# Performance work log

Measured on AMD Instinct MI355X. Metric: run time of the kernel, lower is better.

Reference implementation:

```python
import jax, jax.numpy as jnp
import numpy as np

N, F_IN, F_HID, N_HEADS, F_OUT, ALPHA = 4096, 128, 64, 4, 64, 0.2
AVG_DEG = 32.0


def setup_inputs() -> dict:
    key = jax.random.key(0)
    ks = jax.random.split(key, 8)
    x = jax.random.normal(ks[0], (N, F_IN), dtype=jnp.float32)
    # sparse-ish adjacency (avg degree ~32) + self loops so every row has a neighbor
    adj = (jax.random.uniform(ks[1], (N, N)) < (AVG_DEG / N)).astype(jnp.float32)
    adj = jnp.maximum(adj, jnp.eye(N, dtype=jnp.float32))
    s = 1.0 / np.sqrt(F_IN)
    lin_W = jax.random.uniform(ks[2], (F_IN, F_IN), jnp.float32, -s, s)
    lin_b = jax.random.uniform(ks[3], (F_IN,), jnp.float32, -s, s)
    W_heads = jax.random.normal(ks[4], (N_HEADS, F_IN, F_HID), jnp.float32) * 0.1
    a_heads = jax.random.normal(ks[5], (N_HEADS, 2 * F_HID), jnp.float32) * 0.1
    W_end = jax.random.normal(ks[6], (N_HEADS * F_HID, F_OUT), jnp.float32) * 0.1
    a_end = jax.random.normal(ks[7], (2 * F_OUT,), jnp.float32) * 0.1
    return dict(x=x, adj=adj, lin_W=lin_W, lin_b=lin_b,
                W_heads=W_heads, a_heads=a_heads, W_end=W_end, a_end=a_end)


def _gat_layer(h, adj, W, a):
    # standard dense-masked GAT layer (pyGAT style)
    Wh = h @ W                      # [N, F']
    f = W.shape[1]
    src = Wh @ a[:f]                # [N]  a^T contribution of source node
    dst = Wh @ a[f:]                # [N]  contribution of destination node
    e = jax.nn.leaky_relu(src[:, None] + dst[None, :], ALPHA)  # [N, N]
    e = jnp.where(adj > 0, e, -9e15)
    att = jax.nn.softmax(e, axis=1)  # neighbor softmax per row
    return jax.nn.elu(att @ Wh)      # [N, F']


def reference(x, adj, lin_W, lin_b, W_heads, a_heads, W_end, a_end):
    h = x @ lin_W + lin_b            # nn.Linear(input_features, input_features)
    # parallel multi-head attention, then concat along feature dim
    heads = jax.vmap(lambda W, a: _gat_layer(h, adj, W, a))(W_heads, a_heads)  # [H, N, F_HID]
    hcat = jnp.transpose(heads, (1, 0, 2)).reshape(N, N_HEADS * F_HID)         # [N, H*F_HID]
    out = _gat_layer(hcat, adj, W_end, a_end)                                  # [N, F_OUT]
    return jax.nn.softmax(out, axis=1)
```

## Files before the change

kernel.cpp:

```cpp
#include <hip/hip_runtime.h>

#define GN 4096
#define F_IN 128
#define F_HID 64
#define NHEADS 4
#define F_OUT 64
#define ALPHA 0.2f
#define NGEMM 512

#define OFF_WH     0
#define OFF_SRC1   4194304
#define OFF_DST1   4259840
#define OFF_WH2    4325376
#define OFF_SRC2   5373952
#define OFF_DST2   5390336
#define OFF_BM     5406720

__global__ __launch_bounds__(256) void prep_kernel(
        const float* __restrict__ adj, const float* __restrict__ x,
        const float* __restrict__ linW, const float* __restrict__ linb,
        const float* __restrict__ Wheads, const float* __restrict__ aheads,
        float* __restrict__ Wh, float* __restrict__ src1, float* __restrict__ dst1,
        unsigned short* __restrict__ bm) {
    __shared__ struct { float xs[8][128]; float hs[8][128]; } sm;
    const int tid = threadIdx.x;

    if (blockIdx.x >= NGEMM) {
        const int row = blockIdx.x - NGEMM;
        const float4* a4 = (const float4*)(adj + (size_t)row * GN) + tid * 4;
        float4 v0 = a4[0], v1 = a4[1], v2 = a4[2], v3 = a4[3];
        unsigned msk = 0;
        msk |= (v0.x > 0.0f) ? 1u : 0u;         msk |= (v0.y > 0.0f) ? 2u : 0u;
        msk |= (v0.z > 0.0f) ? 4u : 0u;         msk |= (v0.w > 0.0f) ? 8u : 0u;
        msk |= (v1.x > 0.0f) ? 16u : 0u;        msk |= (v1.y > 0.0f) ? 32u : 0u;
        msk |= (v1.z > 0.0f) ? 64u : 0u;        msk |= (v1.w > 0.0f) ? 128u : 0u;
        msk |= (v2.x > 0.0f) ? 256u : 0u;       msk |= (v2.y > 0.0f) ? 512u : 0u;
        msk |= (v2.z > 0.0f) ? 1024u : 0u;      msk |= (v2.w > 0.0f) ? 2048u : 0u;
        msk |= (v3.x > 0.0f) ? 4096u : 0u;      msk |= (v3.y > 0.0f) ? 8192u : 0u;
        msk |= (v3.z > 0.0f) ? 16384u : 0u;     msk |= (v3.w > 0.0f) ? 32768u : 0u;
        bm[row * 256 + tid] = (unsigned short)msk;
        return;
    }

    const int i0 = blockIdx.x * 8;
    #pragma unroll
    for (int t = 0; t < 4; ++t) {
        int e = t * 256 + tid;
        sm.xs[e >> 7][e & 127] = x[(size_t)i0 * 128 + e];
    }
    __syncthreads();
    {
        const int k = tid & 127;
        const int n0 = tid >> 7;
        float bk = linb[k];
        float a0 = bk, a1 = bk, a2 = bk, a3 = bk;
        for (int j = 0; j < 128; ++j) {
            float w = linW[j * 128 + k];
            a0 += sm.xs[n0][j] * w;
            a1 += sm.xs[n0 + 2][j] * w;
            a2 += sm.xs[n0 + 4][j] * w;
            a3 += sm.xs[n0 + 6][j] * w;
        }
        sm.hs[n0][k] = a0; sm.hs[n0 + 2][k] = a1;
        sm.hs[n0 + 4][k] = a2; sm.hs[n0 + 6][k] = a3;
    }
    __syncthreads();
    {
        const int hd = tid >> 6, f = tid & 63;
        float acc[8] = {0, 0, 0, 0, 0, 0, 0, 0};
        const float* Wp = Wheads + (size_t)hd * F_IN * F_HID + f;
        for (int j = 0; j < 128; ++j) {
            float w = Wp[j * 64];
            #pragma unroll
            for (int n = 0; n < 8; ++n) acc[n] += sm.hs[n][j] * w;
        }
        const float as = aheads[hd * 128 + f];
        const float ad = aheads[hd * 128 + 64 + f];
        #pragma unroll
        for (int n = 0; n < 8; ++n) {
            Wh[(size_t)(i0 + n) * 256 + hd * 64 + f] = acc[n];
            float sv = acc[n] * as, dv = acc[n] * ad;
            #pragma unroll
            for (int o = 32; o > 0; o >>= 1) {
                sv += __shfl_xor(sv, o, 64);
                dv += __shfl_xor(dv, o, 64);
            }
            if (f == 0) { src1[(i0 + n) * 4 + hd] = sv; dst1[(i0 + n) * 4 + hd] = dv; }
        }
    }
}

__device__ __forceinline__ int build_row_nbrs(const unsigned short* __restrict__ bm,
                                              int row, int lane, int* sidx) {
    unsigned long long bits =
        ((const unsigned long long*)(bm + (size_t)row * 256))[lane];
    int c = __popcll(bits);
    int inc = c;
    #pragma unroll
    for (int o = 1; o < 64; o <<= 1) {
        int n = __shfl_up(inc, o, 64);
        if (lane >= o) inc += n;
    }
    int p = inc - c;
    const int deg = __shfl(inc, 63, 64);
    const int col0 = lane * 64;
    while (bits) {
        int k = __ffsll((long long)bits) - 1;
        if (p < 136) sidx[p] = col0 + k;
        ++p;
        bits &= bits - 1;
    }
    const int deg4 = (deg + 3) & ~3;
    if (lane < deg4 - deg) sidx[deg + lane] = 0;
    return deg;
}

__global__ __launch_bounds__(256) void attn_mid_kernel(
        const float* __restrict__ Wh, const float* __restrict__ src1,
        const float* __restrict__ dst1, const float* __restrict__ Wend,
        const float* __restrict__ aend, float* __restrict__ Wh2,
        float* __restrict__ src2, float* __restrict__ dst2,
        const unsigned short* __restrict__ bm) {
    __shared__ float ps[4][528];
    __shared__ float hcat[4][256];
    __shared__ int   sidx[4][136];
    const int wave = threadIdx.x >> 6;
    const int lane = threadIdx.x & 63;
    const int row  = blockIdx.x * 4 + wave;

    const int deg = build_row_nbrs(bm, row, lane, sidx[wave]);
    const int* nb = sidx[wave];
    const int nchunk = (deg + 63) >> 6;

    const float4 s4 = ((const float4*)src1)[row];
    float4 ev[2];
    float4 m4 = make_float4(-1e30f, -1e30f, -1e30f, -1e30f);
    for (int c = 0; c < nchunk; ++c) {
        int t = c * 64 + lane;
        float4 e = make_float4(-1e30f, -1e30f, -1e30f, -1e30f);
        if (t < deg) {
            int j = nb[t];
            float4 d = ((const float4*)dst1)[j];
            e.x = s4.x + d.x; e.x = (e.x > 0.0f) ? e.x : ALPHA * e.x;
            e.y = s4.y + d.y; e.y = (e.y > 0.0f) ? e.y : ALPHA * e.y;
            e.z = s4.z + d.z; e.z = (e.z > 0.0f) ? e.z : ALPHA * e.z;
            e.w = s4.w + d.w; e.w = (e.w > 0.0f) ? e.w : ALPHA * e.w;
        }
        ev[c] = e;
        m4.x = fmaxf(m4.x, e.x); m4.y = fmaxf(m4.y, e.y);
        m4.z = fmaxf(m4.z, e.z); m4.w = fmaxf(m4.w, e.w);
    }
    #pragma unroll
    for (int o = 32; o > 0; o >>= 1) {
        m4.x = fmaxf(m4.x, __shfl_xor(m4.x, o, 64));
        m4.y = fmaxf(m4.y, __shfl_xor(m4.y, o, 64));
        m4.z = fmaxf(m4.z, __shfl_xor(m4.z, o, 64));
        m4.w = fmaxf(m4.w, __shfl_xor(m4.w, o, 64));
    }
    float4 l4 = make_float4(0.f, 0.f, 0.f, 0.f);
    for (int c = 0; c < nchunk; ++c) {
        ev[c].x = expf(ev[c].x - m4.x); l4.x += ev[c].x;
        ev[c].y = expf(ev[c].y - m4.y); l4.y += ev[c].y;
        ev[c].z = expf(ev[c].z - m4.z); l4.z += ev[c].z;
        ev[c].w = expf(ev[c].w - m4.w); l4.w += ev[c].w;
    }
    #pragma unroll
    for (int o = 32; o > 0; o >>= 1) {
        l4.x += __shfl_xor(l4.x, o, 64);
        l4.y += __shfl_xor(l4.y, o, 64);
        l4.z += __shfl_xor(l4.z, o, 64);
        l4.w += __shfl_xor(l4.w, o, 64);
    }
    const float4 inv = make_float4(1.f / l4.x, 1.f / l4.y, 1.f / l4.z, 1.f / l4.w);
    for (int c = 0; c < nchunk; ++c) {
        int t = c * 64 + lane;
        float4 p = make_float4(ev[c].x * inv.x, ev[c].y * inv.y,
                               ev[c].z * inv.z, ev[c].w * inv.w);
        ((float4*)&ps[wave][0])[t] = p;
    }

    const int hl = lane >> 4;
    const float4* Wh4 = (const float4*)Wh;
    float4 acc = make_float4(0.f, 0.f, 0.f, 0.f);
    const int deg4 = (deg + 3) & ~3;
    for (int t = 0; t < deg4; t += 4) {
        int4 jj = *(const int4*)(nb + t);
        float4 w0 = Wh4[(size_t)jj.x * 64 + lane];
        float4 w1 = Wh4[(size_t)jj.y * 64 + lane];
        float4 w2 = Wh4[(size_t)jj.z * 64 + lane];
        float4 w3 = Wh4[(size_t)jj.w * 64 + lane];
        const float* pp = &ps[wave][t * 4 + hl];
        float p0 = pp[0], p1 = pp[4], p2 = pp[8], p3 = pp[12];
        acc.x += p0 * w0.x + p1 * w1.x + p2 * w2.x + p3 * w3.x;
        acc.y += p0 * w0.y + p1 * w1.y + p2 * w2.y + p3 * w3.y;
        acc.z += p0 * w0.z + p1 * w1.z + p2 * w2.z + p3 * w3.z;
        acc.w += p0 * w0.w + p1 * w1.w + p2 * w2.w + p3 * w3.w;
    }
    acc.x = (acc.x > 0.0f) ? acc.x : expm1f(acc.x);
    acc.y = (acc.y > 0.0f) ? acc.y : expm1f(acc.y);
    acc.z = (acc.z > 0.0f) ? acc.z : expm1f(acc.z);
    acc.w = (acc.w > 0.0f) ? acc.w : expm1f(acc.w);
    ((float4*)hcat[wave])[lane] = acc;

    float a0 = 0.f, a1 = 0.f, a2 = 0.f, a3 = 0.f;
    const float* Wp = Wend + lane;
    #pragma unroll 4
    for (int j = 0; j < 256; j += 4) {
        a0 += hcat[wave][j    ] * Wp[(j    ) * 64];
        a1 += hcat[wave][j + 1] * Wp[(j + 1) * 64];
        a2 += hcat[wave][j + 2] * Wp[(j + 2) * 64];
        a3 += hcat[wave][j + 3] * Wp[(j + 3) * 64];
    }
    float aa = (a0 + a1) + (a2 + a3);
    Wh2[(size_t)row * 64 + lane] = aa;
    float s0 = aa * aend[lane], d0 = aa * aend[64 + lane];
    #pragma unroll
    for (int o = 32; o > 0; o >>= 1) {
        s0 += __shfl_xor(s0, o, 64); d0 += __shfl_xor(d0, o, 64);
    }
    if (lane == 0) { src2[row] = s0; dst2[row] = d0; }
}

__global__ __launch_bounds__(256) void attn2_kernel(
        const float* __restrict__ Wh2, const float* __restrict__ src,
        const float* __restrict__ dst, const unsigned short* __restrict__ bm,
        float* __restrict__ out) {
    __shared__ int sidx[4][136];
    const int wave = threadIdx.x >> 6;
    const int lane = threadIdx.x & 63;
    const int row  = blockIdx.x * 4 + wave;

    const int deg = build_row_nbrs(bm, row, lane, sidx[wave]);
    const int* nb = sidx[wave];
    const float s_i = src[row];

    float e[2];
    #pragma unroll
    for (int c = 0; c < 2; ++c) {
        int t = c * 64 + lane;
        float ev = -1e30f;
        if (t < deg) {
            int j = nb[t];
            ev = s_i + dst[j];
            ev = (ev > 0.0f) ? ev : ALPHA * ev;
        }
        e[c] = ev;
    }
    float m = fmaxf(e[0], e[1]);
    #pragma unroll
    for (int o = 32; o > 0; o >>= 1) m = fmaxf(m, __shfl_xor(m, o, 64));
    float l = 0.0f;
    #pragma unroll
    for (int c = 0; c < 2; ++c) { e[c] = expf(e[c] - m); l += e[c]; }
    #pragma unroll
    for (int o = 32; o > 0; o >>= 1) l += __shfl_xor(l, o, 64);

    float accA = 0.0f, accB = 0.0f;
    const float* W2 = Wh2 + lane;
    #pragma unroll
    for (int c = 0; c < 2; ++c) {
        int base = c * 64;
        if (base >= deg) break;
        int nmax = deg - base; if (nmax > 64) nmax = 64;
        int n4 = (nmax + 3) & ~3;
        for (int t = 0; t < n4; t += 4) {
            int4 jj = *(const int4*)(nb + base + t);
            float w0 = W2[(size_t)jj.x * 64];
            float w1 = W2[(size_t)jj.y * 64];
            float w2 = W2[(size_t)jj.z * 64];
            float w3 = W2[(size_t)jj.w * 64];
            float p0 = __shfl(e[c], t, 64),     p1 = __shfl(e[c], t + 1, 64);
            float p2 = __shfl(e[c], t + 2, 64), p3 = __shfl(e[c], t + 3, 64);
            accA += p0 * w0 + p2 * w2;
            accB += p1 * w1 + p3 * w3;
        }
    }
    float v = (accA + accB) / l;
    v = (v > 0.0f) ? v : expm1f(v);

    float mm = v;
    #pragma unroll
    for (int o = 32; o > 0; o >>= 1) mm = fmaxf(mm, __shfl_xor(mm, o, 64));
    float ee = expf(v - mm);
    float ss = ee;
    #pragma unroll
    for (int o = 32; o > 0; o >>= 1) ss += __shfl_xor(ss, o, 64);
    out[(size_t)row * F_OUT + lane] = ee / ss;
}

extern "C" void kernel_launch(void* const* d_in, const int* in_sizes, int n_in,
                              void* d_out, int out_size, void* d_ws, size_t ws_size,
                              hipStream_t stream) {
    const float* x      = (const float*)d_in[0];
    const float* adj    = (const float*)d_in[1];
    const float* lin_W  = (const float*)d_in[2];
    const float* lin_b  = (const float*)d_in[3];
    const float* Wheads = (const float*)d_in[4];
    const float* aheads = (const float*)d_in[5];
    const float* Wend   = (const float*)d_in[6];
    const float* aend   = (const float*)d_in[7];
    float* out = (float*)d_out;

    char* ws = (char*)d_ws;
    float* Wh   = (float*)(ws + OFF_WH);
    float* src1 = (float*)(ws + OFF_SRC1);
    float* dst1 = (float*)(ws + OFF_DST1);
    float* Wh2  = (float*)(ws + OFF_WH2);
    float* src2 = (float*)(ws + OFF_SRC2);
    float* dst2 = (float*)(ws + OFF_DST2);
    unsigned short* bm = (unsigned short*)(ws + OFF_BM);

    prep_kernel<<<NGEMM + GN, 256, 0, stream>>>(adj, x, lin_W, lin_b, Wheads, aheads,
                                                Wh, src1, dst1, bm);
    attn_mid_kernel<<<GN / 4, 256, 0, stream>>>(Wh, src1, dst1, Wend, aend,
                                                Wh2, src2, dst2, bm);
    attn2_kernel<<<GN / 4, 256, 0, stream>>>(Wh2, src2, dst2, bm, out);
}
```

Before: 56.26 us.

## Split mid attention into per-head attention kernel and tiled Wh2 GEMM kernel

The fused per-row attention+projection kernel is split in two. The first assigns one block per row with one wave per head, so each wave runs a scalar softmax and a neighbor gather over its head's 16 float4 columns. The second computes hcat@Wend as a shared-memory tiled GEMM over 8 rows per block, so Wend is reused from shared memory instead of being read per row. In exchange it adds a kernel launch and a global round trip for hcat, plus a cross-lane reduction in the gather.

```diff
diff --git a/kernel.cpp b/kernel.cpp
--- a/kernel.cpp
+++ b/kernel.cpp
@@ -11,10 +11,11 @@
 #define OFF_WH     0
 #define OFF_SRC1   4194304
 #define OFF_DST1   4259840
-#define OFF_WH2    4325376
-#define OFF_SRC2   5373952
-#define OFF_DST2   5390336
-#define OFF_BM     5406720
+#define OFF_HCAT   4325376
+#define OFF_WH2    8519680
+#define OFF_SRC2   9568256
+#define OFF_DST2   9584640
+#define OFF_BM     9601024
 
 __global__ __launch_bounds__(256) void prep_kernel(
         const float* __restrict__ adj, const float* __restrict__ x,
@@ -115,110 +116,118 @@
     return deg;
 }
 
-__global__ __launch_bounds__(256) void attn_mid_kernel(
+__global__ __launch_bounds__(256) void attn1_kernel(
         const float* __restrict__ Wh, const float* __restrict__ src1,
-        const float* __restrict__ dst1, const float* __restrict__ Wend,
-        const float* __restrict__ aend, float* __restrict__ Wh2,
-        float* __restrict__ src2, float* __restrict__ dst2,
-        const unsigned short* __restrict__ bm) {
-    __shared__ float ps[4][528];
-    __shared__ float hcat[4][256];
-    __shared__ int   sidx[4][136];
-    const int wave = threadIdx.x >> 6;
+        const float* __restrict__ dst1, const unsigned short* __restrict__ bm,
+        float* __restrict__ hcat) {
+    __shared__ int   sidx[136];
+    __shared__ int   sdeg;
+    __shared__ float ps[4][136];
+    const int hd   = threadIdx.x >> 6;
     const int lane = threadIdx.x & 63;
-    const int row  = blockIdx.x * 4 + wave;
-
-    const int deg = build_row_nbrs(bm, row, lane, sidx[wave]);
-    const int* nb = sidx[wave];
+    const int row  = blockIdx.x;
+
+    if (hd == 0) {
+        int d = build_row_nbrs(bm, row, lane, sidx);
+        if (lane == 0) sdeg = d;
+    }
+    __syncthreads();
+    const int deg = sdeg;
     const int nchunk = (deg + 63) >> 6;
 
-    const float4 s4 = ((const float4*)src1)[row];
-    float4 ev[2];
-    float4 m4 = make_float4(-1e30f, -1e30f, -1e30f, -1e30f);
+    const float s_i = src1[row * 4 + hd];
+    float e[3];
+    float m = -1e30f;
     for (int c = 0; c < nchunk; ++c) {
         int t = c * 64 + lane;
-        float4 e = make_float4(-1e30f, -1e30f, -1e30f, -1e30f);
+        float ev = -1e30f;
         if (t < deg) {
-            int j = nb[t];
-            float4 d = ((const float4*)dst1)[j];
-            e.x = s4.x + d.x; e.x = (e.x > 0.0f) ? e.x : ALPHA * e.x;
-            e.y = s4.y + d.y; e.y = (e.y > 0.0f) ? e.y : ALPHA * e.y;
-            e.z = s4.z + d.z; e.z = (e.z > 0.0f) ? e.z : ALPHA * e.z;
-            e.w = s4.w + d.w; e.w = (e.w > 0.0f) ? e.w : ALPHA * e.w;
-        }
-        ev[c] = e;
-        m4.x = fmaxf(m4.x, e.x); m4.y = fmaxf(m4.y, e.y);
-        m4.z = fmaxf(m4.z, e.z); m4.w = fmaxf(m4.w, e.w);
-    }
-    #pragma unroll
-    for (int o = 32; o > 0; o >>= 1) {
-        m4.x = fmaxf(m4.x, __shfl_xor(m4.x, o, 64));
-        m4.y = fmaxf(m4.y, __shfl_xor(m4.y, o, 64));
-        m4.z = fmaxf(m4.z, __shfl_xor(m4.z, o, 64));
-        m4.w = fmaxf(m4.w, __shfl_xor(m4.w, o, 64));
-    }
-    float4 l4 = make_float4(0.f, 0.f, 0.f, 0.f);
-    for (int c = 0; c < nchunk; ++c) {
-        ev[c].x = expf(ev[c].x - m4.x); l4.x += ev[c].x;
-        ev[c].y = expf(ev[c].y - m4.y); l4.y += ev[c].y;
-        ev[c].z = expf(ev[c].z - m4.z); l4.z += ev[c].z;
-        ev[c].w = expf(ev[c].w - m4.w); l4.w += ev[c].w;
-    }
-    #pragma unroll
-    for (int o = 32; o > 0; o >>= 1) {
-        l4.x += __shfl_xor(l4.x, o, 64);
-        l4.y += __shfl_xor(l4.y, o, 64);
-        l4.z += __shfl_xor(l4.z, o, 64);
-        l4.w += __shfl_xor(l4.w, o, 64);
-    }
-    const float4 inv = make_float4(1.f / l4.x, 1.f / l4.y, 1.f / l4.z, 1.f / l4.w);
-    for (int c = 0; c < nchunk; ++c) {
-        int t = c * 64 + lane;
-        float4 p = make_float4(ev[c].x * inv.x, ev[c].y * inv.y,
-                               ev[c].z * inv.z, ev[c].w * inv.w);
-        ((float4*)&ps[wave][0])[t] = p;
-    }
-
-    const int hl = lane >> 4;
+            int j = sidx[t];
+            ev = s_i + dst1[j * 4 + hd];
+            ev = (ev > 0.0f) ? ev : ALPHA * ev;
+        }
+        e[c] = ev; m = fmaxf(m, ev);
+    }
+    #pragma unroll
+    for (int o = 32; o > 0; o >>= 1) m = fmaxf(m, __shfl_xor(m, o, 64));
+    float l = 0.0f;
+    for (int c = 0; c < nchunk; ++c) { e[c] = expf(e[c] - m); l += e[c]; }
+    #pragma unroll
+    for (int o = 32; o > 0; o >>= 1) l += __shfl_xor(l, o, 64);
+    const float inv = 1.0f / l;
+    for (int c = 0; c < nchunk; ++c) ps[hd][c * 64 + lane] = e[c] * inv;
+
+    const int q  = lane >> 4;
+    const int f4 = lane & 15;
     const float4* Wh4 = (const float4*)Wh;
     float4 acc = make_float4(0.f, 0.f, 0.f, 0.f);
     const int deg4 = (deg + 3) & ~3;
     for (int t = 0; t < deg4; t += 4) {
-        int4 jj = *(const int4*)(nb + t);
-        float4 w0 = Wh4[(size_t)jj.x * 64 + lane];
-        float4 w1 = Wh4[(size_t)jj.y * 64 + lane];
-        float4 w2 = Wh4[(size_t)jj.z * 64 + lane];
-        float4 w3 = Wh4[(size_t)jj.w * 64 + lane];
-        const float* pp = &ps[wave][t * 4 + hl];
-        float p0 = pp[0], p1 = pp[4], p2 = pp[8], p3 = pp[12];
-        acc.x += p0 * w0.x + p1 * w1.x + p2 * w2.x + p3 * w3.x;
-        acc.y += p0 * w0.y + p1 * w1.y + p2 * w2.y + p3 * w3.y;
-        acc.z += p0 * w0.z + p1 * w1.z + p2 * w2.z + p3 * w3.z;
-        acc.w += p0 * w0.w + p1 * w1.w + p2 * w2.w + p3 * w3.w;
-    }
-    acc.x = (acc.x > 0.0f) ? acc.x : expm1f(acc.x);
-    acc.y = (acc.y > 0.0f) ? acc.y : expm1f(acc.y);
-    acc.z = (acc.z > 0.0f) ? acc.z : expm1f(acc.z);
-    acc.w = (acc.w > 0.0f) ? acc.w : expm1f(acc.w);
-    ((float4*)hcat[wave])[lane] = acc;
-
-    float a0 = 0.f, a1 = 0.f, a2 = 0.f, a3 = 0.f;
-    const float* Wp = Wend + lane;
-    #pragma unroll 4
-    for (int j = 0; j < 256; j += 4) {
-        a0 += hcat[wave][j    ] * Wp[(j    ) * 64];
-        a1 += hcat[wave][j + 1] * Wp[(j + 1) * 64];
-        a2 += hcat[wave][j + 2] * Wp[(j + 2) * 64];
-        a3 += hcat[wave][j + 3] * Wp[(j + 3) * 64];
-    }
-    float aa = (a0 + a1) + (a2 + a3);
-    Wh2[(size_t)row * 64 + lane] = aa;
-    float s0 = aa * aend[lane], d0 = aa * aend[64 + lane];
+        int   j = sidx[t + q];
+        float p = ps[hd][t + q];
+        float4 w = Wh4[(size_t)j * 64 + hd * 16 + f4];
+        acc.x += p * w.x; acc.y += p * w.y; acc.z += p * w.z; acc.w += p * w.w;
+    }
+    #pragma unroll
+    for (int o = 16; o <= 32; o <<= 1) {
+        acc.x += __shfl_xor(acc.x, o, 64);
+        acc.y += __shfl_xor(acc.y, o, 64);
+        acc.z += __shfl_xor(acc.z, o, 64);
+        acc.w += __shfl_xor(acc.w, o, 64);
+    }
+    if (q == 0) {
+        acc.x = (acc.x > 0.0f) ? acc.x : expm1f(acc.x);
+        acc.y = (acc.y > 0.0f) ? acc.y : expm1f(acc.y);
+        acc.z = (acc.z > 0.0f) ? acc.z : expm1f(acc.z);
+        acc.w = (acc.w > 0.0f) ? acc.w : expm1f(acc.w);
+        ((float4*)hcat)[(size_t)row * 64 + hd * 16 + f4] = acc;
+    }
+}
+
+__global__ __launch_bounds__(256) void wh2_kernel(
+        const float* __restrict__ hcat, const float* __restrict__ Wend,
+        const float* __restrict__ aend, float* __restrict__ Wh2,
+        float* __restrict__ src2, float* __restrict__ dst2) {
+    __shared__ float cs[8][256];
+    __shared__ float wt[32][64];
+    const int tid  = threadIdx.x;
+    const int lane = tid & 63;
+    const int n0   = tid >> 6;
+    const int i0   = blockIdx.x * 8;
+    #pragma unroll
+    for (int t = 0; t < 8; ++t) {
+        int e = t * 256 + tid;
+        cs[e >> 8][e & 255] = hcat[(size_t)i0 * 256 + e];
+    }
+    __syncthreads();
+    float a0 = 0.f, a1 = 0.f;
+    for (int tile = 0; tile < 8; ++tile) {
+        const float4* Wsrc = (const float4*)(Wend + tile * 32 * 64);
+        ((float4*)wt)[tid]       = Wsrc[tid];
+        ((float4*)wt)[tid + 256] = Wsrc[tid + 256];
+        __syncthreads();
+        const int jb = tile * 32;
+        #pragma unroll
+        for (int jj = 0; jj < 32; ++jj) {
+            float w = wt[jj][lane];
+            a0 += cs[n0][jb + jj] * w;
+            a1 += cs[n0 + 4][jb + jj] * w;
+        }
+        __syncthreads();
+    }
+    Wh2[(size_t)(i0 + n0) * 64 + lane] = a0;
+    Wh2[(size_t)(i0 + n0 + 4) * 64 + lane] = a1;
+    const float as = aend[lane], ad = aend[64 + lane];
+    float s0 = a0 * as, d0 = a0 * ad, s1 = a1 * as, d1 = a1 * ad;
     #pragma unroll
     for (int o = 32; o > 0; o >>= 1) {
         s0 += __shfl_xor(s0, o, 64); d0 += __shfl_xor(d0, o, 64);
-    }
-    if (lane == 0) { src2[row] = s0; dst2[row] = d0; }
+        s1 += __shfl_xor(s1, o, 64); d1 += __shfl_xor(d1, o, 64);
+    }
+    if (lane == 0) {
+        src2[i0 + n0] = s0;     dst2[i0 + n0] = d0;
+        src2[i0 + n0 + 4] = s1; dst2[i0 + n0 + 4] = d1;
+    }
 }
 
 __global__ __launch_bounds__(256) void attn2_kernel(
@@ -305,6 +314,7 @@
     float* Wh   = (float*)(ws + OFF_WH);
     float* src1 = (float*)(ws + OFF_SRC1);
     float* dst1 = (float*)(ws + OFF_DST1);
+    float* hcat = (float*)(ws + OFF_HCAT);
     float* Wh2  = (float*)(ws + OFF_WH2);
     float* src2 = (float*)(ws + OFF_SRC2);
     float* dst2 = (float*)(ws + OFF_DST2);
@@ -312,7 +322,7 @@
 
     prep_kernel<<<NGEMM + GN, 256, 0, stream>>>(adj, x, lin_W, lin_b, Wheads, aheads,
                                                 Wh, src1, dst1, bm);
-    attn_mid_kernel<<<GN / 4, 256, 0, stream>>>(Wh, src1, dst1, Wend, aend,
-                                                Wh2, src2, dst2, bm);
+    attn1_kernel<<<GN, 256, 0, stream>>>(Wh, src1, dst1, bm, hcat);
+    wh2_kernel<<<GN / 8, 256, 0, stream>>>(hcat, Wend, aend, Wh2, src2, dst2);
     attn2_kernel<<<GN / 4, 256, 0, stream>>>(Wh2, src2, dst2, bm, out);
 }
```

Measured after the change: 60.68 us. +7.9%, slower.
